# Performance work log

Hardware: AMD Instinct MI355X
Metric: run time of the kernel (lower is better)

The kernel has to match this reference:

```python
import jax, jax.numpy as jnp
import numpy as np

N = 768          # nodes
E_HALF = 12288   # undirected edges (both directions added -> E = 24576)
P = 4096         # query pairs
H = 32           # hidden_dim_1wl == hidden_dim_2wl
MAX_X = 100
EPS = 1e-5
LAYER1 = 2


def setup_inputs() -> dict:
    key = jax.random.key(0)
    ks = jax.random.split(key, 12)
    s = 0.1
    x = jax.random.randint(ks[0], (N,), 0, MAX_X + 1)
    half = jax.random.randint(ks[1], (2, E_HALF), 0, N)
    ei = jnp.concatenate([half, half[::-1]], axis=1)          # symmetric edge set [2,E]
    pos = jax.random.randint(ks[2], (P, 2), 0, N)
    emb = jax.random.normal(ks[3], (MAX_X + 1, H)) * s
    gcn_W = jax.random.normal(ks[4], (LAYER1, H, H)) * s
    gcn_b = jnp.zeros((LAYER1, H))
    mlp1_W = jax.random.normal(ks[5], (2 * H, H)) * s
    mlp1_b = jnp.zeros((H,))
    mlp2_W = jax.random.normal(ks[6], (2 * H, H)) * s
    mlp2_b = jnp.zeros((H,))
    mlp3_W = jax.random.normal(ks[7], (H + 1, H)) * s
    mlp3_b = jnp.zeros((H,))
    lin_W = jax.random.normal(ks[8], (2 * H, 1)) * s
    lin_b = jnp.zeros((1,))
    return dict(x=x, ei=ei, pos=pos, emb=emb, gcn_W=gcn_W, gcn_b=gcn_b,
                mlp1_W=mlp1_W, mlp1_b=mlp1_b, mlp2_W=mlp2_W, mlp2_b=mlp2_b,
                mlp3_W=mlp3_W, mlp3_b=mlp3_b, lin_W=lin_W, lin_b=lin_b)


def _graph_norm(h):
    # PyG-style GraphNorm with default params (mean_scale=1, weight=1, bias=0)
    h = h - h.mean(0)
    return h * jax.lax.rsqrt((h * h).mean(0) + EPS)


def reference(x, ei, pos, emb, gcn_W, gcn_b, mlp1_W, mlp1_b,
              mlp2_W, mlp2_b, mlp3_W, mlp3_b, lin_W, lin_b):
    n = x.shape[0]
    d = emb.shape[1]
    h = emb[x]                                                 # [n,H] (dropout=0)
    # --- GCNConv stack: Ahat = D^-1/2 (A+I) D^-1/2 ---
    A = jnp.zeros((n, n), h.dtype).at[ei[0], ei[1]].set(1.0)
    Ahat = A + jnp.eye(n, dtype=h.dtype)
    dinv = jax.lax.rsqrt(Ahat.sum(1))
    An = Ahat * dinv[:, None] * dinv[None, :]
    for l in range(gcn_W.shape[0]):
        h = An @ (h @ gcn_W[l]) + gcn_b[l]
        h = jax.nn.relu(_graph_norm(h))                        # GraphNorm + ReLU
    # --- pair features ---
    xx = h[pos[:, 0]] * h[pos[:, 1]]                           # [P,H]
    val = jnp.concatenate([h[ei[0]], h[ei[1]]], 1)             # [E,2H]
    xe = jax.nn.relu(val @ mlp1_W + mlp1_b)                    # mlps_1
    mul = jax.nn.relu(val @ mlp2_W + mlp2_b)                   # mlps_2[0]
    # --- sparse_bmm as dense [n,n,d] contraction (coalesce sums duplicates -> .add) ---
    Xd = jnp.zeros((n, n, d), h.dtype).at[ei[0], ei[1]].add(xe)
    Md = jnp.zeros((n, n, d), h.dtype).at[ei[0], ei[1]].add(mul)
    C = jnp.einsum('ikd,kjd->ijd', Xd, Md)                     # x_{ij} = sum_k x_{ik}*mul_{kj}
    # support of the sparse result: 2-hop pairs union original edges (sparse_cat)
    adj_b = jnp.zeros((n, n), bool).at[ei[0], ei[1]].set(True)
    af = adj_b.astype(h.dtype)
    mask = ((af @ af) > 0) | adj_b
    ind = af[..., None]                                        # ones-column for original edges
    value = jnp.concatenate([C, ind], -1)                      # [n,n,H+1]
    z = value @ mlp3_W + mlp3_b                                # mlps_3[0]
    # GraphNorm over the edge support only (faithful to sparse values())
    m = mask.astype(h.dtype)[..., None]
    cnt = m.sum()
    mean = (z * m).sum((0, 1)) / cnt
    z = z - mean
    var = ((z * z) * m).sum((0, 1)) / cnt
    z = jax.nn.relu(z * jax.lax.rsqrt(var + EPS))
    # x * sm: multiply by transposed values; zero outside support (= add_zero)
    sym = z * jnp.swapaxes(z, 0, 1) * m
    pair = sym[pos[:, 0], pos[:, 1]]                           # [P,H] (edge_list gather)
    out = jnp.concatenate([pair, xx], 1) @ lin_W + lin_b       # lin_dir -> [P,1]
    return out
```

## Files before the change

kernel.cpp:

```cpp
#include <hip/hip_runtime.h>
#include <hip/hip_bf16.h>

#define NN 768
#define NE 24576
#define NPOS 4096
#define NCELL (NN*NN)
#define NBLK 2304
#define NBLK2 1152
#define NREP 16

typedef __hip_bfloat16 bf16;

__device__ __forceinline__ float ldf(const void* p, int i, int mode) {
    return mode ? __bfloat162float(((const bf16*)p)[i]) : ((const float*)p)[i];
}
__device__ __forceinline__ float aread(float* p) { return atomicAdd(p, 0.f); }
__device__ __forceinline__ int areadi(int* p) { return atomicAdd(p, 0); }

template<int D, int HALF>
__device__ __forceinline__ void redRound(float* v, int lane) {
#pragma unroll
    for (int i = 0; i < HALF; i++) {
        float snd = (lane & D) ? v[i] : v[i + HALF];
        float r = __shfl_xor(snd, D);
        v[i] = ((lane & D) ? v[i + HALF] : v[i]) + r;
    }
}

#define DOT4(Z, A, W) Z += A.x * W.x + A.y * W.y + A.z * W.z + A.w * W.w
#define GATH(rec, q0,q1,q2,q3,q4,q5,q6,q7) { \
    const float4* xr = xep4 + (rec).x * 8; \
    const float4* mr = mulp4 + (rec).y * 8; \
    float4 xv, mv; \
    xv = xr[0]; mv = mr[0]; q0.x += xv.x*mv.x; q0.y += xv.y*mv.y; q0.z += xv.z*mv.z; q0.w += xv.w*mv.w; \
    xv = xr[1]; mv = mr[1]; q1.x += xv.x*mv.x; q1.y += xv.y*mv.y; q1.z += xv.z*mv.z; q1.w += xv.w*mv.w; \
    xv = xr[2]; mv = mr[2]; q2.x += xv.x*mv.x; q2.y += xv.y*mv.y; q2.z += xv.z*mv.z; q2.w += xv.w*mv.w; \
    xv = xr[3]; mv = mr[3]; q3.x += xv.x*mv.x; q3.y += xv.y*mv.y; q3.z += xv.z*mv.z; q3.w += xv.w*mv.w; \
    xv = xr[4]; mv = mr[4]; q4.x += xv.x*mv.x; q4.y += xv.y*mv.y; q4.z += xv.z*mv.z; q4.w += xv.w*mv.w; \
    xv = xr[5]; mv = mr[5]; q5.x += xv.x*mv.x; q5.y += xv.y*mv.y; q5.z += xv.z*mv.z; q5.w += xv.w*mv.w; \
    xv = xr[6]; mv = mr[6]; q6.x += xv.x*mv.x; q6.y += xv.y*mv.y; q6.z += xv.z*mv.z; q6.w += xv.w*mv.w; \
    xv = xr[7]; mv = mr[7]; q7.x += xv.x*mv.x; q7.y += xv.y*mv.y; q7.z += xv.z*mv.z; q7.w += xv.w*mv.w; }

__global__ void k_conv(const void* __restrict__ gW, const void* __restrict__ gB,
                       const void* __restrict__ m1W, const void* __restrict__ m1B,
                       const void* __restrict__ m2W, const void* __restrict__ m2B,
                       const void* __restrict__ m3W, const void* __restrict__ m3B,
                       const void* __restrict__ lW,  const void* __restrict__ lB,
                       const void* __restrict__ emb,
                       float* __restrict__ stats, float* __restrict__ stats1,
                       int* __restrict__ cursor,
                       int* __restrict__ rowlen, int* __restrict__ rtot, int* __restrict__ dcs,
                       int* __restrict__ modeg,
                       float* __restrict__ gwf, float* __restrict__ gbf,
                       float* __restrict__ w1f, float* __restrict__ b1f,
                       float* __restrict__ w2f, float* __restrict__ b2f,
                       float* __restrict__ w3q, float* __restrict__ linf, float* __restrict__ linb) {
    int t = threadIdx.x;
    if (blockIdx.x == 1) {
        for (int i = t; i < NN; i += 256) { cursor[i] = 0; rowlen[i] = 0; rtot[i] = 0; }
        for (int i = t; i < NREP * 80; i += 256) { stats[i] = 0.f; stats1[i] = 0.f; }
        if (t < 8) dcs[t] = 0;
        return;
    }
    __shared__ int bad;
    if (t == 0) bad = 0;
    __syncthreads();
    int local = 0;
    for (int i = t; i < 3232; i += 256) {
        float a = fabsf(__bfloat162float(((const bf16*)emb)[i]));
        if (!(a < 100.f)) local = 1;
    }
    if (local) atomicOr(&bad, 1);
    __syncthreads();
    int mode = bad ? 0 : 1;
    if (t == 0) *modeg = mode;
    for (int i = t; i < 2048; i += 256) {
        gwf[i] = ldf(gW, i, mode);
        w1f[i] = ldf(m1W, i, mode);
        w2f[i] = ldf(m2W, i, mode);
    }
    for (int i = t; i < 64; i += 256) { gbf[i] = ldf(gB, i, mode); linf[i] = ldf(lW, i, mode); }
    if (t < 32) { b1f[t] = ldf(m1B, t, mode); b2f[t] = ldf(m2B, t, mode); }
    for (int i = t; i < 1056; i += 256) { int c = i >> 5, d = i & 31; w3q[d * 36 + c] = ldf(m3W, i, mode); }
    if (t < 32) { w3q[t * 36 + 33] = ldf(m3B, t, mode); w3q[t * 36 + 34] = 0.f; w3q[t * 36 + 35] = 0.f; }
    if (t == 0) linb[0] = ldf(lB, 0, mode);
}

__global__ void k_scatter(const int* __restrict__ ei, int* __restrict__ cell, int* __restrict__ rowlen,
                          int* __restrict__ row_ptr, float* __restrict__ dinv, int* __restrict__ dc) {
    __shared__ int amlast;
    __shared__ int sI[256];
    int t = threadIdx.x;
    int e = blockIdx.x * 256 + t;
    int a = ei[e], b = ei[NE + e];
    if ((unsigned)a < (unsigned)NN && (unsigned)b < (unsigned)NN) {
        int old = atomicAdd(&cell[a * NN + b], 1);
        if (old == 0) atomicAdd(&rowlen[a], 1);
    }
    __syncthreads();
    if (t == 0) { __threadfence(); amlast = (atomicAdd(dc, 1) == 95) ? 1 : 0; }
    __syncthreads();
    if (!amlast) return;
    int i0 = 3 * t;
    int r0 = areadi(&rowlen[i0]), r1 = areadi(&rowlen[i0 + 1]), r2 = areadi(&rowlen[i0 + 2]);
    dinv[i0]     = rsqrtf((float)r0 + 1.f);
    dinv[i0 + 1] = rsqrtf((float)r1 + 1.f);
    dinv[i0 + 2] = rsqrtf((float)r2 + 1.f);
    int s3 = r0 + r1 + r2;
    sI[t] = s3;
    __syncthreads();
    for (int off = 1; off < 256; off <<= 1) {
        int tmp = (t >= off) ? sI[t - off] : 0;
        __syncthreads();
        sI[t] += tmp;
        __syncthreads();
    }
    int excl = sI[t] - s3;
    row_ptr[i0] = excl;
    row_ptr[i0 + 1] = excl + r0;
    row_ptr[i0 + 2] = excl + r0 + r1;
    if (t == 255) row_ptr[NN] = sI[255];
}

__global__ void k_fill(int* __restrict__ cell, const int* __restrict__ row_ptr, int* __restrict__ cursor,
                       int* __restrict__ col_idx, float* __restrict__ cntv, int* __restrict__ pr_row,
                       const int* __restrict__ rowlen, int* __restrict__ rtot,
                       const int* __restrict__ x, const void* __restrict__ emb,
                       const int* __restrict__ modep, float* __restrict__ bufA) {
    int t = threadIdx.x;
    int b = blockIdx.x;
    if (b < NBLK) {
        int idx = b * 256 + t;
        int i = idx / NN;
        int j = idx - i * NN;
        int cv = cell[idx];
        if (cv > 0) {
            int p = row_ptr[i] + atomicAdd(&cursor[i], 1);
            col_idx[p] = j; cntv[p] = (float)cv; pr_row[p] = i;
            cell[idx] = p;
            atomicAdd(&rtot[i], rowlen[j]);
        } else cell[idx] = -1;
    } else {
        int idx = (b - NBLK) * 256 + t;
        int i = idx >> 5, k = idx & 31;
        int xi = x[i]; if (xi < 0) xi = 0; if (xi > 100) xi = 100;
        bufA[idx] = ldf(emb, xi * 32 + k, *modep);
    }
}

__global__ void k_aggmw0(const int* __restrict__ rtot, int* __restrict__ row_base,
                         const int* __restrict__ row_ptr, const int* __restrict__ col_idx,
                         const float* __restrict__ bufA, const float* __restrict__ dinv,
                         const float* __restrict__ gwf, const float* __restrict__ gbf,
                         float* __restrict__ bufB) {
    int t = threadIdx.x;
    if (blockIdx.x == 0) {
        __shared__ int sI[256];
        int r3[3]; int s3 = 0;
#pragma unroll
        for (int q = 0; q < 3; q++) { r3[q] = rtot[3 * t + q]; s3 += r3[q]; }
        sI[t] = s3;
        __syncthreads();
        for (int off = 1; off < 256; off <<= 1) {
            int tmp = (t >= off) ? sI[t - off] : 0;
            __syncthreads();
            sI[t] += tmp;
            __syncthreads();
        }
        int run = sI[t] - s3;
        row_base[3 * t] = run;
        row_base[3 * t + 1] = run + r3[0];
        row_base[3 * t + 2] = run + r3[0] + r3[1];
        return;
    }
    __shared__ float sg[8][32];
    int li = t >> 5, k = t & 31;
    int i = (blockIdx.x - 1) * 8 + li;
    int base = row_ptr[i], len = row_ptr[i + 1] - base;
    float di = dinv[i];
    float acc = di * bufA[i * 32 + k];
    for (int e = 0; e < len; e++) {
        int c = col_idx[base + e];
        acc += dinv[c] * bufA[c * 32 + k];
    }
    sg[li][k] = di * acc;
    __syncthreads();
    int d = k;
    float s = gbf[d];
#pragma unroll
    for (int kk = 0; kk < 32; kk++) s += sg[li][kk] * gwf[kk * 32 + d];
    bufB[i * 32 + d] = s;
}

__global__ void k_hist(const int* __restrict__ row_ptr, const int* __restrict__ col_idx,
                       const int* __restrict__ row_base,
                       int* __restrict__ pcur, int2* __restrict__ paths2, int cap,
                       const float* __restrict__ bufB, float* __restrict__ nrm0) {
    int t = threadIdx.x;
    if (blockIdx.x == NN) {
        __shared__ float r1[256], r2[256];
        int dd = t & 31, g = t >> 5;
        float s = 0.f, s2 = 0.f;
        for (int r = g; r < NN; r += 8) { float v = bufB[r * 32 + dd]; s += v; s2 += v * v; }
        r1[t] = s; r2[t] = s2;
        __syncthreads();
        if (t < 32) {
            float a = 0.f, b2 = 0.f;
            for (int k = 0; k < 8; k++) { a += r1[k * 32 + t]; b2 += r2[k * 32 + t]; }
            float mean = a / (float)NN;
            float var = b2 / (float)NN - mean * mean;
            nrm0[t] = mean;
            nrm0[32 + t] = rsqrtf(fmaxf(var, 0.f) + 1e-5f);
        }
        return;
    }
    __shared__ int hist[NN];
    __shared__ int sc[256];
    int i = blockIdx.x;
    int base = row_ptr[i], len = row_ptr[i + 1] - base;
    int rb = row_base[i];
    int wave = t >> 6, lane = t & 63;
    for (int j = t; j < NN; j += 256) hist[j] = 0;
    __syncthreads();
    for (int ee = wave; ee < len; ee += 4) {
        int k = col_idx[base + ee];
        int kb = row_ptr[k], ke = row_ptr[k + 1];
        for (int e = kb + lane; e < ke; e += 64) atomicAdd(&hist[col_idx[e]], 1);
    }
    __syncthreads();
    int h0 = hist[3 * t], h1 = hist[3 * t + 1], h2 = hist[3 * t + 2];
    int s3 = h0 + h1 + h2;
    sc[t] = s3;
    __syncthreads();
    for (int off = 1; off < 256; off <<= 1) {
        int tmp = (t >= off) ? sc[t - off] : 0;
        __syncthreads();
        sc[t] += tmp;
        __syncthreads();
    }
    int excl = sc[t] - s3;
    int n0 = i * NN + 3 * t;
    pcur[n0]     = rb + excl + h0;
    pcur[n0 + 1] = rb + excl + h0 + h1;
    pcur[n0 + 2] = rb + excl + h0 + h1 + h2;
    hist[3 * t] = excl;
    hist[3 * t + 1] = excl + h0;
    hist[3 * t + 2] = excl + h0 + h1;
    __syncthreads();
    for (int ee = wave; ee < len; ee += 4) {
        int e1 = base + ee;
        int k = col_idx[e1];
        int kb = row_ptr[k], ke = row_ptr[k + 1];
        for (int e = kb + lane; e < ke; e += 64) {
            int j = col_idx[e];
            int slot = rb + atomicAdd(&hist[j], 1);
            if (slot < cap) paths2[slot] = make_int2(e1, e);
        }
    }
}

__global__ void k_aggmw1(const int* __restrict__ row_ptr, const int* __restrict__ col_idx,
                         const float* __restrict__ bufB, const float* __restrict__ nrm0,
                         const float* __restrict__ dinv,
                         const float* __restrict__ gwf, const float* __restrict__ gbf,
                         float* __restrict__ bufA, float* __restrict__ stats1) {
    __shared__ float sg[8][32];
    int t = threadIdx.x;
    int li = t >> 5, k = t & 31;
    int i = blockIdx.x * 8 + li;
    float mk = nrm0[k], rk = nrm0[32 + k];
    int base = row_ptr[i], len = row_ptr[i + 1] - base;
    float di = dinv[i];
    float acc = di * fmaxf((bufB[i * 32 + k] - mk) * rk, 0.f);
    for (int e = 0; e < len; e++) {
        int c = col_idx[base + e];
        acc += dinv[c] * fmaxf((bufB[c * 32 + k] - mk) * rk, 0.f);
    }
    sg[li][k] = di * acc;
    __syncthreads();
    int d = k;
    const float* W = gwf + 1024;
    float s = gbf[32 + d];
#pragma unroll
    for (int kk = 0; kk < 32; kk++) s += sg[li][kk] * W[kk * 32 + d];
    bufA[i * 32 + d] = s;
    __syncthreads();
    sg[li][d] = s;
    __syncthreads();
    if (t < 32) {
        float ps = 0.f, ps2 = 0.f;
#pragma unroll
        for (int q = 0; q < 8; q++) { float v = sg[q][t]; ps += v; ps2 += v * v; }
        float* rep = stats1 + (blockIdx.x & (NREP - 1)) * 80;
        atomicAdd(&rep[t], ps);
        atomicAdd(&rep[32 + t], ps2);
    }
}

__global__ void k_emlp(const float* __restrict__ bufA, const float* __restrict__ stats1,
                       const int* __restrict__ row_ptr, const int* __restrict__ col_idx,
                       const int* __restrict__ pr_row, const float* __restrict__ cntv,
                       const float* __restrict__ w1f, const float* __restrict__ b1f,
                       const float* __restrict__ w2f, const float* __restrict__ b2f,
                       float* __restrict__ xep, float* __restrict__ mulp, float* __restrict__ h) {
    __shared__ float nmean[32], nrstd[32];
    int t = threadIdx.x;
    int b = blockIdx.x;
    if (t < 32) {
        float s = 0.f, s2 = 0.f;
#pragma unroll
        for (int r = 0; r < NREP; r++) { s += stats1[r * 80 + t]; s2 += stats1[r * 80 + 32 + t]; }
        float mean = s / (float)NN;
        float var = s2 / (float)NN - mean * mean;
        nmean[t] = mean;
        nrstd[t] = rsqrtf(fmaxf(var, 0.f) + 1e-5f);
    }
    __syncthreads();
    if (b < 3072) {
        int d = t & 31;
        int p = b * 8 + (t >> 5);
        if (p >= row_ptr[NN]) {
            if (p < NE) { xep[p * 32 + d] = 0.f; mulp[p * 32 + d] = 0.f; }
            return;
        }
        int i = pr_row[p], j = col_idx[p];
        float a1 = b1f[d], a2 = b2f[d];
#pragma unroll
        for (int c = 0; c < 32; c++) {
            float hv = fmaxf((bufA[i * 32 + c] - nmean[c]) * nrstd[c], 0.f);
            a1 += hv * w1f[c * 32 + d];
            a2 += hv * w2f[c * 32 + d];
        }
#pragma unroll
        for (int c = 0; c < 32; c++) {
            float hv = fmaxf((bufA[j * 32 + c] - nmean[c]) * nrstd[c], 0.f);
            a1 += hv * w1f[(32 + c) * 32 + d];
            a2 += hv * w2f[(32 + c) * 32 + d];
        }
        float cv = cntv[p];
        xep[p * 32 + d]  = cv * fmaxf(a1, 0.f);
        mulp[p * 32 + d] = cv * fmaxf(a2, 0.f);
    } else {
        int idx = (b - 3072) * 256 + t;
        int d = idx & 31;
        h[idx] = fmaxf((bufA[idx] - nmean[d]) * nrstd[d], 0.f);
    }
}

__global__ __launch_bounds__(256, 3) void k_big(const int* __restrict__ pcur,
                                                const int2* __restrict__ paths2,
                                                const int* __restrict__ cell,
                                                const float4* __restrict__ xep4, const float4* __restrict__ mulp4,
                                                const float* __restrict__ w3q,
                                                float* __restrict__ stats, int* __restrict__ done,
                                                float* __restrict__ nrm, int cap) {
    __shared__ float sS1[32], sS2[32];
    __shared__ float sCm;
    __shared__ int amlast;
    int t = threadIdx.x, lane = t & 63;
    int b = blockIdx.x;
    int n0 = b * 512 + 2 * t;
    if (t == 0) sCm = 0.f;
    if (t < 32) { sS1[t] = 0.f; sS2[t] = 0.f; }
    __syncthreads();
    int p0a = (n0 == 0) ? 0 : pcur[n0 - 1];
    int p1a = pcur[n0];
    int p1b = pcur[n0 + 1];
    if (p0a > cap) p0a = cap; if (p1a > cap) p1a = cap; if (p1b > cap) p1b = cap;
    int lenA = p1a - p0a, lenB = p1b - p1a;
    int lim = (lenA > lenB) ? lenA : lenB;
    float4 a0 = {0.f,0.f,0.f,0.f}, a1 = a0, a2 = a0, a3 = a0, a4 = a0, a5 = a0, a6 = a0, a7 = a0;
    float4 c0 = a0, c1 = a0, c2 = a0, c3 = a0, c4 = a0, c5 = a0, c6 = a0, c7 = a0;
    for (int q = 0; q < lim; q++) {
        int2 recA, recB;
        bool doA = q < lenA, doB = q < lenB;
        if (doA) recA = paths2[p0a + q];
        if (doB) recB = paths2[p1a + q];
        if (doA) GATH(recA, a0, a1, a2, a3, a4, a5, a6, a7);
        if (doB) GATH(recB, c0, c1, c2, c3, c4, c5, c6, c7);
    }
    bool adja = cell[n0] >= 0;
    bool adjb = cell[n0 + 1] >= 0;
    float afa = adja ? 1.f : 0.f;
    float afb = adjb ? 1.f : 0.f;
    float mska = (lenA > 0 || adja) ? 1.f : 0.f;
    float mskb = (lenB > 0 || adjb) ? 1.f : 0.f;
#pragma unroll
    for (int ch = 0; ch < 2; ch++) {
        float v[32];
#pragma unroll
        for (int j = 0; j < 16; j++) {
            int dd = ch * 16 + j;
            const float4* wr = (const float4*)(w3q + dd * 36);
            float4 wv = wr[8];
            float za = wv.y + afa * wv.x;
            float zb = wv.y + afb * wv.x;
            wv = wr[0]; DOT4(za, a0, wv); DOT4(zb, c0, wv);
            wv = wr[1]; DOT4(za, a1, wv); DOT4(zb, c1, wv);
            wv = wr[2]; DOT4(za, a2, wv); DOT4(zb, c2, wv);
            wv = wr[3]; DOT4(za, a3, wv); DOT4(zb, c3, wv);
            wv = wr[4]; DOT4(za, a4, wv); DOT4(zb, c4, wv);
            wv = wr[5]; DOT4(za, a5, wv); DOT4(zb, c5, wv);
            wv = wr[6]; DOT4(za, a6, wv); DOT4(zb, c6, wv);
            wv = wr[7]; DOT4(za, a7, wv); DOT4(zb, c7, wv);
            v[j] = mska * za + mskb * zb;
            v[16 + j] = mska * za * za + mskb * zb * zb;
        }
#pragma unroll
        for (int i2 = 0; i2 < 32; i2++) v[i2] += __shfl_xor(v[i2], 32);
        redRound<16, 16>(v, lane);
        redRound<8, 8>(v, lane);
        redRound<4, 4>(v, lane);
        redRound<2, 2>(v, lane);
        redRound<1, 1>(v, lane);
        if (lane < 32) {
            if (lane < 16) atomicAdd(&sS1[ch * 16 + lane], v[0]);
            else           atomicAdd(&sS2[ch * 16 + lane - 16], v[0]);
        }
    }
    {
        float cm2 = mska + mskb;
        for (int off = 32; off >= 1; off >>= 1) cm2 += __shfl_xor(cm2, off);
        if (lane == 0) atomicAdd(&sCm, cm2);
    }
    __syncthreads();
    float* srep = stats + (b & (NREP - 1)) * 80;
    if (t < 32) {
        atomicAdd(&srep[t], sS1[t]);
        atomicAdd(&srep[32 + t], sS2[t]);
    }
    if (t == 32) atomicAdd(&srep[64], sCm);
    __syncthreads();
    if (t == 0) {
        __threadfence();
        amlast = (atomicAdd(done, 1) == NBLK2 - 1) ? 1 : 0;
    }
    __syncthreads();
    if (amlast && t < 32) {
        float sum1 = 0.f, sum2 = 0.f;
        for (int r = 0; r < NREP; r++) {
            sum1 += aread(&stats[r * 80 + t]);
            sum2 += aread(&stats[r * 80 + 32 + t]);
        }
        float cmv = 0.f;
        for (int r = 0; r < NREP; r++) cmv += aread(&stats[r * 80 + 64]);
        if (cmv < 1.f) cmv = 1.f;
        float mean = sum1 / cmv;
        float var = sum2 / cmv - mean * mean;
        nrm[t] = mean;
        nrm[32 + t] = rsqrtf(fmaxf(var, 0.f) + 1e-5f);
    }
}

__global__ void k_out(const int* __restrict__ pos, const int* __restrict__ pcur,
                      const int2* __restrict__ paths2,
                      const int* __restrict__ cell,
                      const float* __restrict__ xep, const float* __restrict__ mulp,
                      const float* __restrict__ h,
                      const float* __restrict__ w3q,
                      const float* __restrict__ nrm,
                      const float* __restrict__ linf, const float* __restrict__ linb,
                      const int* __restrict__ modep, int cap, void* __restrict__ outp) {
    __shared__ float Cb[4][2][32];
    int t = threadIdx.x;
    int w = t >> 6, lane = t & 63, d = lane & 31, dir = lane >> 5;
    int p = blockIdx.x * 4 + w;
    int a = pos[2 * p], b = pos[2 * p + 1];
    if ((unsigned)a >= (unsigned)NN) a = 0;
    if ((unsigned)b >= (unsigned)NN) b = 0;
    int r = dir ? b : a;
    int cc = dir ? a : b;
    int n = r * NN + cc;
    int p1 = pcur[n];
    int p0 = (n == 0) ? 0 : pcur[n - 1];
    if (p0 > cap) p0 = cap; if (p1 > cap) p1 = cap;
    float acc = 0.f;
    for (int q = p0; q < p1; q++) {
        int2 rec = paths2[q];
        acc += xep[rec.x * 32 + d] * mulp[rec.y * 32 + d];
    }
    Cb[w][dir][d] = acc;
    bool adj = cell[n] >= 0;
    float msk = (p1 > p0 || adj) ? 1.f : 0.f;
    __syncthreads();
    float z = w3q[d * 36 + 33] + (adj ? 1.f : 0.f) * w3q[d * 36 + 32];
#pragma unroll
    for (int c = 0; c < 32; c++) z += Cb[w][dir][c] * w3q[d * 36 + c];
    float zn = fmaxf((z - nrm[d]) * nrm[32 + d], 0.f);
    float zp = __shfl_xor(zn, 32);
    float symd = msk * zn * zp;
    float xxd = h[a * 32 + d] * h[b * 32 + d];
    float contrib = symd * linf[d] + xxd * linf[32 + d];
    for (int off = 16; off >= 1; off >>= 1) contrib += __shfl_xor(contrib, off);
    if (lane == 0) {
        float v = contrib + linb[0];
        v = fminf(fmaxf(v, -1e4f), 1e4f);
        if (*modep) ((bf16*)outp)[p] = __float2bfloat16(v);
        else        ((float*)outp)[p] = v;
    }
}

extern "C" void kernel_launch(void* const* d_in, const int* in_sizes, int n_in,
                              void* d_out, int out_size, void* d_ws, size_t ws_size,
                              hipStream_t stream) {
    const void* px  = d_in[0];  const void* pei = d_in[1];  const void* ppos = d_in[2];
    const void* pemb = d_in[3]; const void* pgW = d_in[4];  const void* pgB  = d_in[5];
    const void* pm1W = d_in[6]; const void* pm1B = d_in[7]; const void* pm2W = d_in[8];
    const void* pm2B = d_in[9]; const void* pm3W = d_in[10]; const void* pm3B = d_in[11];
    const void* plW = d_in[12]; const void* plB = d_in[13];
    {
        int c2048 = 0, c64 = 0, c32 = 0;
        for (int i = 0; i < n_in; i++) {
            int s = in_sizes[i]; const void* p = d_in[i];
            switch (s) {
                case 768:   px = p; break;
                case 49152: pei = p; break;
                case 8192:  ppos = p; break;
                case 3232:  pemb = p; break;
                case 2048:  if (c2048 == 0) pgW = p; else if (c2048 == 1) pm1W = p; else pm2W = p; c2048++; break;
                case 64:    if (c64 == 0) pgB = p; else plW = p; c64++; break;
                case 32:    if (c32 == 0) pm1B = p; else if (c32 == 1) pm2B = p; else pm3B = p; c32++; break;
                case 1056:  pm3W = p; break;
                case 1:     plB = p; break;
                default: break;
            }
        }
    }

    char* ws = (char*)d_ws;
    size_t off = 0;
    auto alloc = [&](size_t bytes) -> void* {
        void* pp = ws + off;
        off += (bytes + 255) & ~(size_t)255;
        return pp;
    };
    int*   cell    = (int*)alloc(NCELL * 4);
    int*   pcur    = (int*)alloc(NCELL * 4);
    int*   rowlen  = (int*)alloc(NN * 4);
    int*   rtot    = (int*)alloc(NN * 4);
    int*   row_base= (int*)alloc(NN * 4);
    int*   row_ptr = (int*)alloc((NN + 1) * 4);
    int*   col_idx = (int*)alloc(NE * 4);
    float* cntv    = (float*)alloc(NE * 4);
    int*   pr_row  = (int*)alloc(NE * 4);
    int*   cursor  = (int*)alloc(NN * 4);
    float* dinv    = (float*)alloc(NN * 4);
    float* h       = (float*)alloc(NN * 32 * 4);
    float* bufA    = (float*)alloc(NN * 32 * 4);
    float* bufB    = (float*)alloc(NN * 32 * 4);
    float* xep     = (float*)alloc(NE * 32 * 4);
    float* mulp    = (float*)alloc(NE * 32 * 4);
    float* stats   = (float*)alloc(NREP * 80 * 4);
    float* stats1  = (float*)alloc(NREP * 80 * 4);
    float* nrm     = (float*)alloc(64 * 4);
    float* nrm0    = (float*)alloc(64 * 4);
    float* gwf     = (float*)alloc(2048 * 4);
    float* gbf     = (float*)alloc(64 * 4);
    float* w1f     = (float*)alloc(2048 * 4);
    float* b1f     = (float*)alloc(32 * 4);
    float* w2f     = (float*)alloc(2048 * 4);
    float* b2f     = (float*)alloc(32 * 4);
    float* w3q     = (float*)alloc(32 * 36 * 4);
    float* linf    = (float*)alloc(64 * 4);
    float* linb    = (float*)alloc(4);
    int*   modeg   = (int*)alloc(4);
    int*   dcs     = (int*)alloc(8 * 4);
    size_t remain = (ws_size > off) ? (ws_size - off) : 0;
    int cap = (int)(remain / 8);
    if (cap > (1 << 20)) cap = (1 << 20);
    int2*  paths2  = (int2*)alloc((size_t)cap * 8);

    hipMemsetAsync(cell, 0, (size_t)NCELL * 4, stream);
    k_conv<<<2, 256, 0, stream>>>(pgW, pgB, pm1W, pm1B, pm2W, pm2B, pm3W, pm3B, plW, plB,
                                  pemb, stats, stats1, cursor, rowlen, rtot, dcs, modeg,
                                  gwf, gbf, w1f, b1f, w2f, b2f, w3q, linf, linb);
    k_scatter<<<96, 256, 0, stream>>>((const int*)pei, cell, rowlen, row_ptr, dinv, &dcs[0]);
    k_fill<<<NBLK + 96, 256, 0, stream>>>(cell, row_ptr, cursor, col_idx, cntv, pr_row,
                                          rowlen, rtot, (const int*)px, pemb, modeg, bufA);
    k_aggmw0<<<1 + 96, 256, 0, stream>>>(rtot, row_base, row_ptr, col_idx, bufA, dinv, gwf, gbf, bufB);
    k_hist<<<NN + 1, 256, 0, stream>>>(row_ptr, col_idx, row_base, pcur, paths2, cap, bufB, nrm0);
    k_aggmw1<<<96, 256, 0, stream>>>(row_ptr, col_idx, bufB, nrm0, dinv, gwf, gbf, bufA, stats1);
    k_emlp<<<3072 + 96, 256, 0, stream>>>(bufA, stats1, row_ptr, col_idx, pr_row, cntv,
                                          w1f, b1f, w2f, b2f, xep, mulp, h);
    k_big<<<NBLK2, 256, 0, stream>>>(pcur, paths2, cell, (const float4*)xep, (const float4*)mulp,
                                     w3q, stats, &dcs[1], nrm, cap);
    k_out<<<NPOS / 4, 256, 0, stream>>>((const int*)ppos, pcur, paths2, cell, xep, mulp, h,
                                        w3q, nrm, linf, linb, modeg, cap, d_out);
}
```

Before: 307.9 us.

## Merge weight-convert kernel into scatter, memset aux buffers, batch gather loads

The separate k_conv launch is removed. Its weight conversion moves into an extra block of k_scatter, and its zeroing of counters and stats becomes a single hipMemsetAsync over a contiguous aux region, so one kernel launch and its serialization are gone. The GATH macro now issues all sixteen float4 loads before the multiply-adds to expose more memory-level parallelism. k_big's launch bounds drop from 3 to 2 waves per SIMD, giving more registers for the extra live loads at the cost of occupancy.

Measured after the change: 299.8 us. 1.03x faster.

```diff
diff --git a/kernel.cpp b/kernel.cpp
--- a/kernel.cpp
+++ b/kernel.cpp
@@ -28,69 +28,63 @@
 }
 
 #define DOT4(Z, A, W) Z += A.x * W.x + A.y * W.y + A.z * W.z + A.w * W.w
+
 #define GATH(rec, q0,q1,q2,q3,q4,q5,q6,q7) { \
     const float4* xr = xep4 + (rec).x * 8; \
     const float4* mr = mulp4 + (rec).y * 8; \
-    float4 xv, mv; \
-    xv = xr[0]; mv = mr[0]; q0.x += xv.x*mv.x; q0.y += xv.y*mv.y; q0.z += xv.z*mv.z; q0.w += xv.w*mv.w; \
-    xv = xr[1]; mv = mr[1]; q1.x += xv.x*mv.x; q1.y += xv.y*mv.y; q1.z += xv.z*mv.z; q1.w += xv.w*mv.w; \
-    xv = xr[2]; mv = mr[2]; q2.x += xv.x*mv.x; q2.y += xv.y*mv.y; q2.z += xv.z*mv.z; q2.w += xv.w*mv.w; \
-    xv = xr[3]; mv = mr[3]; q3.x += xv.x*mv.x; q3.y += xv.y*mv.y; q3.z += xv.z*mv.z; q3.w += xv.w*mv.w; \
-    xv = xr[4]; mv = mr[4]; q4.x += xv.x*mv.x; q4.y += xv.y*mv.y; q4.z += xv.z*mv.z; q4.w += xv.w*mv.w; \
-    xv = xr[5]; mv = mr[5]; q5.x += xv.x*mv.x; q5.y += xv.y*mv.y; q5.z += xv.z*mv.z; q5.w += xv.w*mv.w; \
-    xv = xr[6]; mv = mr[6]; q6.x += xv.x*mv.x; q6.y += xv.y*mv.y; q6.z += xv.z*mv.z; q6.w += xv.w*mv.w; \
-    xv = xr[7]; mv = mr[7]; q7.x += xv.x*mv.x; q7.y += xv.y*mv.y; q7.z += xv.z*mv.z; q7.w += xv.w*mv.w; }
-
-__global__ void k_conv(const void* __restrict__ gW, const void* __restrict__ gB,
-                       const void* __restrict__ m1W, const void* __restrict__ m1B,
-                       const void* __restrict__ m2W, const void* __restrict__ m2B,
-                       const void* __restrict__ m3W, const void* __restrict__ m3B,
-                       const void* __restrict__ lW,  const void* __restrict__ lB,
-                       const void* __restrict__ emb,
-                       float* __restrict__ stats, float* __restrict__ stats1,
-                       int* __restrict__ cursor,
-                       int* __restrict__ rowlen, int* __restrict__ rtot, int* __restrict__ dcs,
-                       int* __restrict__ modeg,
-                       float* __restrict__ gwf, float* __restrict__ gbf,
-                       float* __restrict__ w1f, float* __restrict__ b1f,
-                       float* __restrict__ w2f, float* __restrict__ b2f,
-                       float* __restrict__ w3q, float* __restrict__ linf, float* __restrict__ linb) {
-    int t = threadIdx.x;
-    if (blockIdx.x == 1) {
-        for (int i = t; i < NN; i += 256) { cursor[i] = 0; rowlen[i] = 0; rtot[i] = 0; }
-        for (int i = t; i < NREP * 80; i += 256) { stats[i] = 0.f; stats1[i] = 0.f; }
-        if (t < 8) dcs[t] = 0;
+    float4 xv0 = xr[0], xv1 = xr[1], xv2 = xr[2], xv3 = xr[3]; \
+    float4 xv4 = xr[4], xv5 = xr[5], xv6 = xr[6], xv7 = xr[7]; \
+    float4 mv0 = mr[0], mv1 = mr[1], mv2 = mr[2], mv3 = mr[3]; \
+    float4 mv4 = mr[4], mv5 = mr[5], mv6 = mr[6], mv7 = mr[7]; \
+    q0.x += xv0.x*mv0.x; q0.y += xv0.y*mv0.y; q0.z += xv0.z*mv0.z; q0.w += xv0.w*mv0.w; \
+    q1.x += xv1.x*mv1.x; q1.y += xv1.y*mv1.y; q1.z += xv1.z*mv1.z; q1.w += xv1.w*mv1.w; \
+    q2.x += xv2.x*mv2.x; q2.y += xv2.y*mv2.y; q2.z += xv2.z*mv2.z; q2.w += xv2.w*mv2.w; \
+    q3.x += xv3.x*mv3.x; q3.y += xv3.y*mv3.y; q3.z += xv3.z*mv3.z; q3.w += xv3.w*mv3.w; \
+    q4.x += xv4.x*mv4.x; q4.y += xv4.y*mv4.y; q4.z += xv4.z*mv4.z; q4.w += xv4.w*mv4.w; \
+    q5.x += xv5.x*mv5.x; q5.y += xv5.y*mv5.y; q5.z += xv5.z*mv5.z; q5.w += xv5.w*mv5.w; \
+    q6.x += xv6.x*mv6.x; q6.y += xv6.y*mv6.y; q6.z += xv6.z*mv6.z; q6.w += xv6.w*mv6.w; \
+    q7.x += xv7.x*mv7.x; q7.y += xv7.y*mv7.y; q7.z += xv7.z*mv7.z; q7.w += xv7.w*mv7.w; }
+
+__global__ void k_scatter(const int* __restrict__ ei, int* __restrict__ cell, int* __restrict__ rowlen,
+                          int* __restrict__ row_ptr, float* __restrict__ dinv, int* __restrict__ dc,
+                          const void* __restrict__ gW, const void* __restrict__ gB,
+                          const void* __restrict__ m1W, const void* __restrict__ m1B,
+                          const void* __restrict__ m2W, const void* __restrict__ m2B,
+                          const void* __restrict__ m3W, const void* __restrict__ m3B,
+                          const void* __restrict__ lW,  const void* __restrict__ lB,
+                          const void* __restrict__ emb, int* __restrict__ modeg,
+                          float* __restrict__ gwf, float* __restrict__ gbf,
+                          float* __restrict__ w1f, float* __restrict__ b1f,
+                          float* __restrict__ w2f, float* __restrict__ b2f,
+                          float* __restrict__ w3q, float* __restrict__ linf, float* __restrict__ linb) {
+    int t = threadIdx.x;
+    if (blockIdx.x == 96) {
+        __shared__ int bad;
+        if (t == 0) bad = 0;
+        __syncthreads();
+        int local = 0;
+        for (int i = t; i < 3232; i += 256) {
+            float a = fabsf(__bfloat162float(((const bf16*)emb)[i]));
+            if (!(a < 100.f)) local = 1;
+        }
+        if (local) atomicOr(&bad, 1);
+        __syncthreads();
+        int mode = bad ? 0 : 1;
+        if (t == 0) *modeg = mode;
+        for (int i = t; i < 2048; i += 256) {
+            gwf[i] = ldf(gW, i, mode);
+            w1f[i] = ldf(m1W, i, mode);
+            w2f[i] = ldf(m2W, i, mode);
+        }
+        for (int i = t; i < 64; i += 256) { gbf[i] = ldf(gB, i, mode); linf[i] = ldf(lW, i, mode); }
+        if (t < 32) { b1f[t] = ldf(m1B, t, mode); b2f[t] = ldf(m2B, t, mode); }
+        for (int i = t; i < 1056; i += 256) { int c = i >> 5, d = i & 31; w3q[d * 36 + c] = ldf(m3W, i, mode); }
+        if (t < 32) { w3q[t * 36 + 33] = ldf(m3B, t, mode); w3q[t * 36 + 34] = 0.f; w3q[t * 36 + 35] = 0.f; }
+        if (t == 0) linb[0] = ldf(lB, 0, mode);
         return;
     }
-    __shared__ int bad;
-    if (t == 0) bad = 0;
-    __syncthreads();
-    int local = 0;
-    for (int i = t; i < 3232; i += 256) {
-        float a = fabsf(__bfloat162float(((const bf16*)emb)[i]));
-        if (!(a < 100.f)) local = 1;
-    }
-    if (local) atomicOr(&bad, 1);
-    __syncthreads();
-    int mode = bad ? 0 : 1;
-    if (t == 0) *modeg = mode;
-    for (int i = t; i < 2048; i += 256) {
-        gwf[i] = ldf(gW, i, mode);
-        w1f[i] = ldf(m1W, i, mode);
-        w2f[i] = ldf(m2W, i, mode);
-    }
-    for (int i = t; i < 64; i += 256) { gbf[i] = ldf(gB, i, mode); linf[i] = ldf(lW, i, mode); }
-    if (t < 32) { b1f[t] = ldf(m1B, t, mode); b2f[t] = ldf(m2B, t, mode); }
-    for (int i = t; i < 1056; i += 256) { int c = i >> 5, d = i & 31; w3q[d * 36 + c] = ldf(m3W, i, mode); }
-    if (t < 32) { w3q[t * 36 + 33] = ldf(m3B, t, mode); w3q[t * 36 + 34] = 0.f; w3q[t * 36 + 35] = 0.f; }
-    if (t == 0) linb[0] = ldf(lB, 0, mode);
-}
-
-__global__ void k_scatter(const int* __restrict__ ei, int* __restrict__ cell, int* __restrict__ rowlen,
-                          int* __restrict__ row_ptr, float* __restrict__ dinv, int* __restrict__ dc) {
     __shared__ int amlast;
     __shared__ int sI[256];
-    int t = threadIdx.x;
     int e = blockIdx.x * 256 + t;
     int a = ei[e], b = ei[NE + e];
     if ((unsigned)a < (unsigned)NN && (unsigned)b < (unsigned)NN) {
@@ -347,7 +341,7 @@
     }
 }
 
-__global__ __launch_bounds__(256, 3) void k_big(const int* __restrict__ pcur,
+__global__ __launch_bounds__(256, 2) void k_big(const int* __restrict__ pcur,
                                                 const int2* __restrict__ paths2,
                                                 const int* __restrict__ cell,
                                                 const float4* __restrict__ xep4, const float4* __restrict__ mulp4,
@@ -536,22 +530,25 @@
     };
     int*   cell    = (int*)alloc(NCELL * 4);
     int*   pcur    = (int*)alloc(NCELL * 4);
+    char*  aux0    = ws + off;
     int*   rowlen  = (int*)alloc(NN * 4);
     int*   rtot    = (int*)alloc(NN * 4);
+    int*   cursor  = (int*)alloc(NN * 4);
+    float* stats   = (float*)alloc(NREP * 80 * 4);
+    float* stats1  = (float*)alloc(NREP * 80 * 4);
+    int*   dcs     = (int*)alloc(8 * 4);
+    size_t auxlen  = (ws + off) - aux0;
     int*   row_base= (int*)alloc(NN * 4);
     int*   row_ptr = (int*)alloc((NN + 1) * 4);
     int*   col_idx = (int*)alloc(NE * 4);
     float* cntv    = (float*)alloc(NE * 4);
     int*   pr_row  = (int*)alloc(NE * 4);
-    int*   cursor  = (int*)alloc(NN * 4);
     float* dinv    = (float*)alloc(NN * 4);
     float* h       = (float*)alloc(NN * 32 * 4);
     float* bufA    = (float*)alloc(NN * 32 * 4);
     float* bufB    = (float*)alloc(NN * 32 * 4);
     float* xep     = (float*)alloc(NE * 32 * 4);
     float* mulp    = (float*)alloc(NE * 32 * 4);
-    float* stats   = (float*)alloc(NREP * 80 * 4);
-    float* stats1  = (float*)alloc(NREP * 80 * 4);
     float* nrm     = (float*)alloc(64 * 4);
     float* nrm0    = (float*)alloc(64 * 4);
     float* gwf     = (float*)alloc(2048 * 4);
@@ -564,17 +561,16 @@
     float* linf    = (float*)alloc(64 * 4);
     float* linb    = (float*)alloc(4);
     int*   modeg   = (int*)alloc(4);
-    int*   dcs     = (int*)alloc(8 * 4);
     size_t remain = (ws_size > off) ? (ws_size - off) : 0;
     int cap = (int)(remain / 8);
     if (cap > (1 << 20)) cap = (1 << 20);
     int2*  paths2  = (int2*)alloc((size_t)cap * 8);
 
     hipMemsetAsync(cell, 0, (size_t)NCELL * 4, stream);
-    k_conv<<<2, 256, 0, stream>>>(pgW, pgB, pm1W, pm1B, pm2W, pm2B, pm3W, pm3B, plW, plB,
-                                  pemb, stats, stats1, cursor, rowlen, rtot, dcs, modeg,
-                                  gwf, gbf, w1f, b1f, w2f, b2f, w3q, linf, linb);
-    k_scatter<<<96, 256, 0, stream>>>((const int*)pei, cell, rowlen, row_ptr, dinv, &dcs[0]);
+    hipMemsetAsync(aux0, 0, auxlen, stream);
+    k_scatter<<<97, 256, 0, stream>>>((const int*)pei, cell, rowlen, row_ptr, dinv, &dcs[0],
+                                      pgW, pgB, pm1W, pm1B, pm2W, pm2B, pm3W, pm3B, plW, plB,
+                                      pemb, modeg, gwf, gbf, w1f, b1f, w2f, b2f, w3q, linf, linb);
     k_fill<<<NBLK + 96, 256, 0, stream>>>(cell, row_ptr, cursor, col_idx, cntv, pr_row,
                                           rowlen, rtot, (const int*)px, pemb, modeg, bufA);
     k_aggmw0<<<1 + 96, 256, 0, stream>>>(rtot, row_base, row_ptr, col_idx, bufA, dinv, gwf, gbf, bufB);
```
